# Performance work log

Measured on AMD Instinct MI355X. Metric: run time of the kernel, lower is better.

Reference implementation:

```python
import jax, jax.numpy as jnp
import numpy as np

GRAPH_BIAS_SCALE = 0.7
COMMITMENT_COST = 0.25
DECAY = 0.995
EPS = 1e-6

N_TOKENS = 32768
LATENT = 512
N_SYMBOLS = 8192
EMBED_DIM = 2 * LATENT


def setup_inputs() -> dict:
    key = jax.random.key(0)
    ks = jax.random.split(key, 6)
    return {
        "z_real": jax.random.normal(ks[0], (N_TOKENS, LATENT), jnp.float32),
        "z_imag": jax.random.normal(ks[1], (N_TOKENS, LATENT), jnp.float32),
        "prev_symbol_idx": jax.random.randint(ks[2], (N_TOKENS,), 0, N_SYMBOLS, jnp.int64),
        "codebook": jax.random.normal(ks[3], (N_SYMBOLS, EMBED_DIM), jnp.float32),
        "cluster_size": jax.random.uniform(ks[4], (N_SYMBOLS,), jnp.float32),
        "embed_avg": jax.random.normal(ks[5], (N_SYMBOLS, EMBED_DIM), jnp.float32),
        "adjacency": jax.random.normal(jax.random.fold_in(key, 7), (N_SYMBOLS, N_SYMBOLS), jnp.float32),
    }


def reference(z_real, z_imag, prev_symbol_idx, codebook, cluster_size, embed_avg, adjacency):
    n_symbols = codebook.shape[0]
    z_flat = jnp.concatenate([z_real, z_imag], axis=-1)  # [N, 2*latent]

    # squared-distance matrix via matmul expansion: [N, n_symbols]
    d = (jnp.sum(z_flat ** 2, axis=1, keepdims=True)
         + jnp.sum(codebook ** 2, axis=1)
         - 2.0 * z_flat @ codebook.T)

    # graph-adjacency prior bias (row gather + sigmoid)
    bias = GRAPH_BIAS_SCALE * jax.nn.sigmoid(adjacency[prev_symbol_idx])
    d = d - bias

    min_indices = jnp.argmin(d, axis=1)          # [N]
    z_q = codebook[min_indices]                  # gather, pre-EMA codebook

    # --- EMA codebook update (training mode), scatter via segment_sum ---
    ones = jnp.ones(min_indices.shape, jnp.float32)
    counts = jax.ops.segment_sum(ones, min_indices, num_segments=n_symbols)
    new_cluster_size = cluster_size * DECAY + counts * (1.0 - DECAY)
    embed_sum = jax.ops.segment_sum(jax.lax.stop_gradient(z_flat), min_indices,
                                    num_segments=n_symbols)
    new_embed_avg = embed_avg * DECAY + embed_sum * (1.0 - DECAY)
    n_total = jnp.sum(new_cluster_size)
    cs = (new_cluster_size + EPS) / (n_total + n_symbols * EPS) * n_total
    new_codebook = new_embed_avg / cs[:, None]

    # --- losses and straight-through estimator ---
    loss_vq = jnp.mean((z_q - jax.lax.stop_gradient(z_flat)) ** 2)
    loss_commit = jnp.mean((jax.lax.stop_gradient(z_q) - z_flat) ** 2)
    loss = loss_vq + COMMITMENT_COST * loss_commit

    z_q_st = z_flat + jax.lax.stop_gradient(z_q - z_flat)
    D = z_real.shape[-1]
    z_complex = jax.lax.complex(z_q_st[..., :D], z_q_st[..., D:])

    return z_complex, loss, min_indices, new_codebook, new_cluster_size, new_embed_avg
```

## Files before the change

### kernel.cpp

```cpp
#include <hip/hip_runtime.h>
#include <math.h>
#include <float.h>

#define M_TOK   32768
#define NSYM    8192
#define KDIM    1024
#define LAT     512

#define DECAY_F 0.995f
#define OMD_F   0.005f
#define GBS_F   0.7f
#define EPS_F   1e-6f
#define WIN_F   2.5f
#define LOSS_SCALE (1.25f / 33554432.0f)

typedef unsigned short u16;
typedef unsigned int   u32;
typedef short short8 __attribute__((ext_vector_type(8)));
typedef float f32x4  __attribute__((ext_vector_type(4)));

#define GLOAD_LDS16(g, l) \
    __builtin_amdgcn_global_load_lds((const __attribute__((address_space(1))) u32*)(g), \
                                     (__attribute__((address_space(3))) u32*)(l), 16, 0, 0)

__device__ __forceinline__ u16 f2bf(float f) {
    u32 u = __float_as_uint(f);
    return (u16)((u + 0x7FFF + ((u >> 16) & 1)) >> 16);
}

__global__ void k_conv(const float* __restrict__ zr, const float* __restrict__ zi,
                       const float* __restrict__ cb,
                       u16* __restrict__ A, u16* __restrict__ B,
                       float* __restrict__ cnorm,
                       u32* __restrict__ counts, u32* __restrict__ cursors,
                       u32* __restrict__ qcount, float* __restrict__ out_loss) {
    const int bid = blockIdx.x;
    if (bid < 16384) {
        size_t t = (size_t)bid * 256 + threadIdx.x;
        size_t base = t * 8;
        int tok = (int)(base >> 10);
        int k0  = (int)(base & 1023);
        const float* src = (k0 < 512) ? zr + (size_t)tok * 512 + k0
                                      : zi + (size_t)tok * 512 + (k0 - 512);
        float4 f0 = *(const float4*)src;
        float4 f1 = *(const float4*)(src + 4);
        u32 q0 = f2bf(f0.x) | ((u32)f2bf(f0.y) << 16);
        u32 q1 = f2bf(f0.z) | ((u32)f2bf(f0.w) << 16);
        u32 q2 = f2bf(f1.x) | ((u32)f2bf(f1.y) << 16);
        u32 q3 = f2bf(f1.z) | ((u32)f2bf(f1.w) << 16);
        *(uint4*)&A[base] = make_uint4(q0, q1, q2, q3);
    } else if (bid < 20480) {
        const int b2 = bid - 16384;
        size_t t = (size_t)b2 * 256 + threadIdx.x;
        size_t base = t * 8;
        float4 f0 = *(const float4*)&cb[base];
        float4 f1 = *(const float4*)&cb[base + 4];
        u32 q0 = f2bf(f0.x) | ((u32)f2bf(f0.y) << 16);
        u32 q1 = f2bf(f0.z) | ((u32)f2bf(f0.w) << 16);
        u32 q2 = f2bf(f1.x) | ((u32)f2bf(f1.y) << 16);
        u32 q3 = f2bf(f1.z) | ((u32)f2bf(f1.w) << 16);
        *(uint4*)&B[base] = make_uint4(q0, q1, q2, q3);
        float nrm = f0.x * f0.x + f0.y * f0.y + f0.z * f0.z + f0.w * f0.w
                  + f1.x * f1.x + f1.y * f1.y + f1.z * f1.z + f1.w * f1.w;
#pragma unroll
        for (int m = 32; m; m >>= 1) nrm += __shfl_xor(nrm, m, 64);
        __shared__ float part[4];
        int lane = threadIdx.x & 63, w = threadIdx.x >> 6;
        if (lane == 0) part[w] = nrm;
        __syncthreads();
        if (threadIdx.x == 0)   cnorm[b2 * 2]     = part[0] + part[1];
        if (threadIdx.x == 128) cnorm[b2 * 2 + 1] = part[2] + part[3];
    } else {
        int i = (bid - 20480) * 256 + threadIdx.x;
        if (i < NSYM) { counts[i] = 0; cursors[i] = 0; }
        if (i == 0) { qcount[0] = 0; out_loss[0] = 0.0f; }
    }
}

__global__ __launch_bounds__(256, 4) void k_screen(
    const u16* __restrict__ Ah, const u16* __restrict__ Bh,
    const float* __restrict__ cnorm,
    float* __restrict__ candV, u16* __restrict__ candI)
{
    __shared__ __align__(16) unsigned char smA[16384];
    __shared__ __align__(16) unsigned char smB[16384];
    __shared__ float smv[128][2][2];
    __shared__ float smi[128][2];

    const int sblk = (blockIdx.x & 7) * 128 + (blockIdx.x >> 3);
    const int bx = sblk >> 2;
    const int by = sblk & 3;

    const int tid  = threadIdx.x;
    const int lane = tid & 63;
    const int w    = tid >> 6;
    const int wr   = w >> 1, wc = w & 1;
    const int row0 = bx * 128;
    const int sBase = w * 256;

    for (int cc = 0; cc < 16; ++cc) {
        const int chunk = by * 16 + cc;
        const int colBase = chunk * 128;

        f32x4 acc[4][4];
#pragma unroll
        for (int m = 0; m < 4; ++m)
#pragma unroll
            for (int n = 0; n < 4; ++n) acc[m][n] = (f32x4){0.f, 0.f, 0.f, 0.f};

        for (int ks = 0; ks < 16; ++ks) {
            const int kk0 = ks * 64;
            __syncthreads();
#pragma unroll
            for (int i = 0; i < 4; ++i) {
                int slot = sBase + i * 64 + lane;
                int r = slot >> 3;
                int c = (slot & 7) ^ (r & 7);
                const u16* ga = Ah + ((size_t)(row0 + r) * KDIM + kk0 + c * 8);
                GLOAD_LDS16(ga, smA + (size_t)(sBase + i * 64) * 16);
                const u16* gb = Bh + ((size_t)(colBase + r) * KDIM + kk0 + c * 8);
                GLOAD_LDS16(gb, smB + (size_t)(sBase + i * 64) * 16);
            }
            __syncthreads();
#pragma unroll
            for (int h = 0; h < 2; ++h) {
                short8 af[4], bfr[4];
#pragma unroll
                for (int m = 0; m < 4; ++m) {
                    int r = wr * 64 + m * 16 + (lane & 15);
                    int byte = r * 128 + h * 64 + (lane >> 4) * 16;
                    byte ^= (r & 7) << 4;
                    af[m] = *(const short8*)(smA + byte);
                }
#pragma unroll
                for (int n = 0; n < 4; ++n) {
                    int r = wc * 64 + n * 16 + (lane & 15);
                    int byte = r * 128 + h * 64 + (lane >> 4) * 16;
                    byte ^= (r & 7) << 4;
                    bfr[n] = *(const short8*)(smB + byte);
                }
#pragma unroll
                for (int m = 0; m < 4; ++m)
#pragma unroll
                    for (int n = 0; n < 4; ++n)
                        acc[m][n] = __builtin_amdgcn_mfma_f32_16x16x32_bf16(
                            af[m], bfr[n], acc[m][n], 0, 0, 0);
            }
        }

        float cn[4];
#pragma unroll
        for (int n = 0; n < 4; ++n)
            cn[n] = cnorm[colBase + wc * 64 + n * 16 + (lane & 15)];

#pragma unroll
        for (int m = 0; m < 4; ++m)
#pragma unroll
            for (int j = 0; j < 4; ++j) {
                int rowL = wr * 64 + m * 16 + (lane >> 4) * 4 + j;
                float v1 = INFINITY, v2 = INFINITY, i1v = 0.f;
#pragma unroll
                for (int n = 0; n < 4; ++n) {
                    float s = cn[n] - 2.0f * acc[m][n][j];
                    float ci = (float)(colBase + wc * 64 + n * 16 + (lane & 15));
                    if (s < v1) { v2 = v1; v1 = s; i1v = ci; }
                    else v2 = fminf(v2, s);
                }
#pragma unroll
                for (int msk = 1; msk < 16; msk <<= 1) {
                    float o1 = __shfl_xor(v1, msk, 16);
                    float oi = __shfl_xor(i1v, msk, 16);
                    float o2 = __shfl_xor(v2, msk, 16);
                    float n2 = fminf(fminf(v2, o2), fmaxf(v1, o1));
                    if (o1 < v1) { v1 = o1; i1v = oi; }
                    v2 = n2;
                }
                if ((lane & 15) == 0) {
                    smv[rowL][wc][0] = v1;  smv[rowL][wc][1] = v2;
                    smi[rowL][wc] = i1v;
                }
            }
        __syncthreads();
        {
            int half = tid >> 7;
            int row  = tid & 127;
            float v1 = smv[row][half][0], v2 = smv[row][half][1];
            float iv = smi[row][half];
            size_t tcol = (size_t)(row0 + row);
            int halfIdx = chunk * 2 + half;
            candV[(size_t)(halfIdx * 2 + 0) * M_TOK + tcol] = v1;
            candV[(size_t)(halfIdx * 2 + 1) * M_TOK + tcol] = v2;
            candI[(size_t)halfIdx * M_TOK + tcol]           = (u16)iv;
        }
    }
}

__global__ void k_zero(u32* __restrict__ counts, u32* __restrict__ cursors,
                       u32* __restrict__ qcount, float* __restrict__ out_loss) {
    int i = blockIdx.x * 256 + threadIdx.x;
    if (i < NSYM) { counts[i] = 0; cursors[i] = 0; }
    if (i == 0) { out_loss[0] = 0.0f; qcount[0] = 0; }
}

__device__ __forceinline__ void rescore(
    const float* __restrict__ codebook, const float* __restrict__ adjacency,
    const double* zreg, int prw, int col, int lane, double& bestS, int& bestI)
{
    const float* crow = codebook + (size_t)col * KDIM;
    double dot = 0.0, cn2 = 0.0;
#pragma unroll
    for (int j = 0; j < 16; ++j) {
        double c = (double)crow[lane + 64 * j];
        dot += c * zreg[j]; cn2 += c * c;
    }
#pragma unroll
    for (int m = 32; m; m >>= 1) {
        dot += __shfl_xor(dot, m, 64);
        cn2 += __shfl_xor(cn2, m, 64);
    }
    double a = (double)adjacency[(size_t)prw * NSYM + col];
    double sc = cn2 - 2.0 * dot - (double)GBS_F / (1.0 + exp(-a));
    if (sc < bestS || (sc == bestS && col < bestI)) { bestS = sc; bestI = col; }
}

#define SEL_TOK 32
__global__ __launch_bounds__(256) void k_select(
    const float* __restrict__ zr, const float* __restrict__ zi,
    const int* __restrict__ prev,
    const float* __restrict__ codebook,
    const float* __restrict__ adjacency,
    const float* __restrict__ candV, const u16* __restrict__ candI,
    float* __restrict__ out_idx, u32* __restrict__ counts,
    u32* __restrict__ qcount, u32* __restrict__ queue)
{
    __shared__ float sv[256][SEL_TOK + 1];
    __shared__ u16   si[128][SEL_TOK + 2];
    const int tok0 = blockIdx.x * SEL_TOK;
    const int w = threadIdx.x >> 6, lane = threadIdx.x & 63;

    for (int idx = threadIdx.x; idx < 256 * SEL_TOK; idx += 256) {
        int e = idx >> 5, t = idx & (SEL_TOK - 1);
        sv[e][t] = candV[(size_t)e * M_TOK + tok0 + t];
    }
    for (int idx = threadIdx.x; idx < 128 * SEL_TOK; idx += 256) {
        int e = idx >> 5, t = idx & (SEL_TOK - 1);
        si[e][t] = candI[(size_t)e * M_TOK + tok0 + t];
    }
    __syncthreads();

    for (int tt = 0; tt < SEL_TOK / 4; ++tt) {
        const int t = w * (SEL_TOK / 4) + tt;
        const int tok = tok0 + t;
        float va1 = sv[4 * lane + 0][t];
        float va2 = sv[4 * lane + 1][t];
        float vb1 = sv[4 * lane + 2][t];
        float vb2 = sv[4 * lane + 3][t];
        int   ia  = (int)si[2 * lane + 0][t];
        int   ib  = (int)si[2 * lane + 1][t];

        float mm = fminf(va1, vb1);
#pragma unroll
        for (int m = 32; m; m >>= 1) mm = fminf(mm, __shfl_xor(mm, m, 64));
        const float thr = mm + WIN_F;

        unsigned long long m1a = __ballot(va1 <= thr);
        unsigned long long m1b = __ballot(vb1 <= thr);
        unsigned long long mh  = __ballot(va2 <= thr) | __ballot(vb2 <= thr);

        if (mh != 0) {
            if (lane == 0) { u32 q = atomicAdd(qcount, 1u); queue[q] = (u32)tok; }
        } else if (__popcll(m1a) + __popcll(m1b) == 1) {
            int bestI;
            if (m1a) { int c = __ffsll(m1a) - 1; bestI = __shfl(ia, c, 64); }
            else     { int c = __ffsll(m1b) - 1; bestI = __shfl(ib, c, 64); }
            if (lane == 0) {
                out_idx[tok] = (float)bestI;
                atomicAdd(&counts[bestI], 1u);
            }
        } else {
            double zreg[16];
#pragma unroll
            for (int j = 0; j < 8; ++j)
                zreg[j] = (double)zr[(size_t)tok * LAT + lane + 64 * j];
#pragma unroll
            for (int j = 0; j < 8; ++j)
                zreg[8 + j] = (double)zi[(size_t)tok * LAT + lane + 64 * j];
            const int prw = prev[tok];
            double bestS = DBL_MAX; int bestI = 0x7FFFFFFF;
            unsigned long long sa = m1a, sb = m1b;
            while (sa) { int c = __ffsll(sa) - 1; sa &= sa - 1;
                rescore(codebook, adjacency, zreg, prw, __shfl(ia, c, 64), lane, bestS, bestI); }
            while (sb) { int c = __ffsll(sb) - 1; sb &= sb - 1;
                rescore(codebook, adjacency, zreg, prw, __shfl(ib, c, 64), lane, bestS, bestI); }
            if (lane == 0) {
                out_idx[tok] = (float)bestI;
                atomicAdd(&counts[bestI], 1u);
            }
        }
    }
}

#define MAXC 384
__global__ __launch_bounds__(256) void k_rescan(
    const float* __restrict__ zr, const float* __restrict__ zi,
    const int* __restrict__ prev,
    const float* __restrict__ codebook,
    const float* __restrict__ adjacency,
    const float* __restrict__ candV, const u16* __restrict__ candI,
    const u32* __restrict__ qcount, const u32* __restrict__ queue,
    float* __restrict__ out_idx, u32* __restrict__ counts)
{
    __shared__ double zd[KDIM];
    __shared__ float v1h[128], v2h[128];
    __shared__ u16   i1h[128];
    __shared__ int   collist[MAXC];
    __shared__ int   nsing_sh, nh_sh, scanall_sh;
    __shared__ int   halves[128];
    __shared__ double wsc[4];
    __shared__ int    wix[4];
    __shared__ float  mm_sh;

    const int tid = threadIdx.x;
    const int w = tid >> 6, lane = tid & 63;
    const u32 nq = qcount[0];

    for (u32 qi = blockIdx.x; qi < nq; qi += gridDim.x) {
        const int tok = (int)queue[qi];

        if (tid < 128) {
            v1h[tid] = candV[(size_t)(tid * 2 + 0) * M_TOK + tok];
            v2h[tid] = candV[(size_t)(tid * 2 + 1) * M_TOK + tok];
            i1h[tid] = candI[(size_t)tid * M_TOK + tok];
        }
        for (int k = tid; k < LAT; k += 256) {
            zd[k]       = (double)zr[(size_t)tok * LAT + k];
            zd[LAT + k] = (double)zi[(size_t)tok * LAT + k];
        }
        if (tid == 0) { nsing_sh = 0; nh_sh = 0; scanall_sh = 0; }
        __syncthreads();

        if (tid < 64) {
            float m = fminf(v1h[tid], v1h[tid + 64]);
#pragma unroll
            for (int s = 32; s; s >>= 1) m = fminf(m, __shfl_xor(m, s, 64));
            if (tid == 0) mm_sh = m;
        }
        __syncthreads();
        const float thr = mm_sh + WIN_F;

        if (tid < 128) {
            bool hs = (v2h[tid] <= thr);
            if (hs) { int p = atomicAdd(&nh_sh, 1); halves[p] = tid; }
            else if (v1h[tid] <= thr) { int p = atomicAdd(&nsing_sh, 1); collist[p] = (int)i1h[tid]; }
        }
        __syncthreads();
        int nsing = nsing_sh, nh = nh_sh;
        int nc = nsing + nh * 64;
        if (nc > MAXC) { if (tid == 0) scanall_sh = 1; }
        __syncthreads();
        if (!scanall_sh) {
            for (int h = 0; h < nh; ++h) {
                if (tid < 64) collist[nsing + h * 64 + tid] = halves[h] * 64 + tid;
            }
            nc = nsing + nh * 64;
        }
        __syncthreads();

        const int prw = prev[tok];
        double bestS = DBL_MAX; int bestI = 0x7FFFFFFF;
        const int total = scanall_sh ? NSYM : nc;
        for (int ci = w; ci < total; ci += 4) {
            int col = scanall_sh ? ci : collist[ci];
            const float* crow = codebook + (size_t)col * KDIM;
            double dot = 0.0, cn2 = 0.0;
#pragma unroll
            for (int j = 0; j < 16; ++j) {
                double c = (double)crow[lane + 64 * j];
                dot += c * zd[lane + 64 * j]; cn2 += c * c;
            }
#pragma unroll
            for (int s = 32; s; s >>= 1) {
                dot += __shfl_xor(dot, s, 64);
                cn2 += __shfl_xor(cn2, s, 64);
            }
            double a = (double)adjacency[(size_t)prw * NSYM + col];
            double sc = cn2 - 2.0 * dot - (double)GBS_F / (1.0 + exp(-a));
            if (sc < bestS || (sc == bestS && col < bestI)) { bestS = sc; bestI = col; }
        }
        if (lane == 0) { wsc[w] = bestS; wix[w] = bestI; }
        __syncthreads();
        if (tid == 0) {
            double bs = wsc[0]; int bi = wix[0];
#pragma unroll
            for (int q = 1; q < 4; ++q) {
                if (wsc[q] < bs || (wsc[q] == bs && wix[q] < bi)) { bs = wsc[q]; bi = wix[q]; }
            }
            out_idx[tok] = (float)bi;
            atomicAdd(&counts[bi], 1u);
        }
        __syncthreads();
    }
}

__global__ __launch_bounds__(1024) void k_scan(
    const u32* __restrict__ counts, const float* __restrict__ cs_old,
    float* __restrict__ out_cs, u32* __restrict__ offsets,
    float* __restrict__ scal)
{
    const int tid = threadIdx.x;
    const int lane = tid & 63, w = tid >> 6;
    const int base = tid * 8;
    u32 c[8], pre[8], T = 0;
#pragma unroll
    for (int q = 0; q < 8; ++q) { c[q] = counts[base + q]; pre[q] = T; T += c[q]; }
    u32 inc = T;
#pragma unroll
    for (int d = 1; d < 64; d <<= 1) {
        u32 v = __shfl_up(inc, d, 64);
        if (lane >= d) inc += v;
    }
    __shared__ u32 wt[16];
    if (lane == 63) wt[w] = inc;
    __syncthreads();
    if (tid < 16) {
        u32 v = wt[tid];
#pragma unroll
        for (int d = 1; d < 16; d <<= 1) {
            u32 o = __shfl_up(v, d, 16);
            if (tid >= d) v += o;
        }
        wt[tid] = v;
    }
    __syncthreads();
    u32 ex = (w ? wt[w - 1] : 0) + inc - T;
#pragma unroll
    for (int q = 0; q < 8; ++q) offsets[base + q] = ex + pre[q];

    float nt = 0.0f;
#pragma unroll
    for (int q = 0; q < 8; ++q) {
        float ncs = cs_old[base + q] * DECAY_F + OMD_F * (float)c[q];
        out_cs[base + q] = ncs;
        nt += ncs;
    }
#pragma unroll
    for (int m = 32; m; m >>= 1) nt += __shfl_xor(nt, m, 64);
    __shared__ float red[16];
    if (lane == 0) red[w] = nt;
    __syncthreads();
    if (tid == 0) {
        float s = 0.0f;
#pragma unroll
        for (int i = 0; i < 16; ++i) s += red[i];
        scal[0] = s;
        scal[1] = s + (float)NSYM * EPS_F;
    }
}

__global__ void k_place(const float* __restrict__ idxf, const u32* __restrict__ offsets,
                        u32* __restrict__ cursors, u32* __restrict__ list) {
    int t = blockIdx.x * 256 + threadIdx.x;
    int s = (int)idxf[t];
    u32 slot = atomicAdd(&cursors[s], 1u);
    list[offsets[s] + slot] = (u32)t;
}

__global__ __launch_bounds__(256) void k_emit_fused(
    const float* __restrict__ zr, const float* __restrict__ zi,
    const float* __restrict__ codebook, const float* __restrict__ embed_avg,
    const u32* __restrict__ counts, const u32* __restrict__ offsets,
    const u32* __restrict__ list, const float* __restrict__ out_cs,
    const float* __restrict__ scal,
    float* __restrict__ out_ea, float* __restrict__ out_cb,
    float* __restrict__ out_zc, float* __restrict__ out_loss, int interleaved)
{
    const int s = blockIdx.x;
    const u32 cnt = counts[s], off = offsets[s];
    const int g = threadIdx.x >> 7;
    const int j = (threadIdx.x & 127) * 4;
    float4 cbr = *(const float4*)&codebook[(size_t)s * KDIM + j];
    float4 cbi = *(const float4*)&codebook[(size_t)s * KDIM + LAT + j];
    float ar0 = 0.f, ar1 = 0.f, ar2 = 0.f, ar3 = 0.f;
    float ai0 = 0.f, ai1 = 0.f, ai2 = 0.f, ai3 = 0.f;
    float lsum = 0.f;
    for (u32 n = g; n < cnt; n += 2) {
        int t = (int)list[off + n];
        float4 z0 = *(const float4*)&zr[(size_t)t * LAT + j];
        float4 z1 = *(const float4*)&zi[(size_t)t * LAT + j];
        ar0 += z0.x; ar1 += z0.y; ar2 += z0.z; ar3 += z0.w;
        ai0 += z1.x; ai1 += z1.y; ai2 += z1.z; ai3 += z1.w;
        if (interleaved) {
            float2* dst = (float2*)out_zc + (size_t)t * LAT + j;
            dst[0] = make_float2(cbr.x, cbi.x); dst[1] = make_float2(cbr.y, cbi.y);
            dst[2] = make_float2(cbr.z, cbi.z); dst[3] = make_float2(cbr.w, cbi.w);
        } else {
            *(float4*)&out_zc[(size_t)t * LAT + j] = cbr;
        }
        float d;
        d = cbr.x - z0.x; lsum += d * d;  d = cbr.y - z0.y; lsum += d * d;
        d = cbr.z - z0.z; lsum += d * d;  d = cbr.w - z0.w; lsum += d * d;
        d = cbi.x - z1.x; lsum += d * d;  d = cbi.y - z1.y; lsum += d * d;
        d = cbi.z - z1.z; lsum += d * d;  d = cbi.w - z1.w; lsum += d * d;
    }
    __shared__ float comb[128][8];
    if (g == 1) {
        int r = threadIdx.x & 127;
        comb[r][0] = ar0; comb[r][1] = ar1; comb[r][2] = ar2; comb[r][3] = ar3;
        comb[r][4] = ai0; comb[r][5] = ai1; comb[r][6] = ai2; comb[r][7] = ai3;
    }
    __syncthreads();
    if (g == 0) {
        int r = threadIdx.x;
        ar0 += comb[r][0]; ar1 += comb[r][1]; ar2 += comb[r][2]; ar3 += comb[r][3];
        ai0 += comb[r][4]; ai1 += comb[r][5]; ai2 += comb[r][6]; ai3 += comb[r][7];
        float4 ea0 = *(const float4*)&embed_avg[(size_t)s * KDIM + j];
        float4 ea1 = *(const float4*)&embed_avg[(size_t)s * KDIM + LAT + j];
        float4 ner = make_float4(ea0.x * DECAY_F + ar0 * OMD_F, ea0.y * DECAY_F + ar1 * OMD_F,
                                 ea0.z * DECAY_F + ar2 * OMD_F, ea0.w * DECAY_F + ar3 * OMD_F);
        float4 nei = make_float4(ea1.x * DECAY_F + ai0 * OMD_F, ea1.y * DECAY_F + ai1 * OMD_F,
                                 ea1.z * DECAY_F + ai2 * OMD_F, ea1.w * DECAY_F + ai3 * OMD_F);
        *(float4*)&out_ea[(size_t)s * KDIM + j]       = ner;
        *(float4*)&out_ea[(size_t)s * KDIM + LAT + j] = nei;
        float ntot = scal[0], denom = scal[1];
        float cs = (out_cs[s] + EPS_F) / denom * ntot;
        float inv = 1.0f / cs;
        *(float4*)&out_cb[(size_t)s * KDIM + j] =
            make_float4(ner.x * inv, ner.y * inv, ner.z * inv, ner.w * inv);
        *(float4*)&out_cb[(size_t)s * KDIM + LAT + j] =
            make_float4(nei.x * inv, nei.y * inv, nei.z * inv, nei.w * inv);
    }
#pragma unroll
    for (int m = 32; m; m >>= 1) lsum += __shfl_xor(lsum, m, 64);
    __shared__ float red[4];
    int wv = threadIdx.x >> 6, lane = threadIdx.x & 63;
    if (lane == 0) red[wv] = lsum;
    __syncthreads();
    if (threadIdx.x == 0)
        atomicAdd(out_loss, (red[0] + red[1] + red[2] + red[3]) * LOSS_SCALE);
}

__global__ __launch_bounds__(256) void k_emit(
    const float* __restrict__ zr, const float* __restrict__ zi,
    const float* __restrict__ embed_avg,
    const u32* __restrict__ counts, const u32* __restrict__ offsets,
    const u32* __restrict__ list, const float* __restrict__ out_cs,
    const float* __restrict__ scal,
    float* __restrict__ out_ea, float* __restrict__ out_cb)
{
    const int s = blockIdx.x;
    const u32 cnt = counts[s], off = offsets[s];
    const int j = threadIdx.x * 4;
    float a0 = 0.f, a1 = 0.f, a2 = 0.f, a3 = 0.f;
    for (u32 n = 0; n < cnt; ++n) {
        int t = (int)list[off + n];
        const float* src = (j < 512) ? zr + (size_t)t * 512 + j
                                     : zi + (size_t)t * 512 + (j - 512);
        float4 v = *(const float4*)src;
        a0 += v.x; a1 += v.y; a2 += v.z; a3 += v.w;
    }
    float4 ea = *(const float4*)&embed_avg[(size_t)s * KDIM + j];
    float4 nea = make_float4(ea.x * DECAY_F + a0 * OMD_F,
                             ea.y * DECAY_F + a1 * OMD_F,
                             ea.z * DECAY_F + a2 * OMD_F,
                             ea.w * DECAY_F + a3 * OMD_F);
    *(float4*)&out_ea[(size_t)s * KDIM + j] = nea;
    float ntot = scal[0], denom = scal[1];
    float cs = (out_cs[s] + EPS_F) / denom * ntot;
    float inv = 1.0f / cs;
    *(float4*)&out_cb[(size_t)s * KDIM + j] =
        make_float4(nea.x * inv, nea.y * inv, nea.z * inv, nea.w * inv);
}

__global__ __launch_bounds__(256) void k_zq(
    const float* __restrict__ zr, const float* __restrict__ zi,
    const float* __restrict__ codebook, const float* __restrict__ idxf,
    float* __restrict__ out_zc, float* __restrict__ out_loss, int interleaved)
{
    const int w = threadIdx.x >> 6, lane = threadIdx.x & 63;
    const int tok = blockIdx.x * 4 + w;
    const int mi = (int)idxf[tok];
    const int j0 = lane * 8;
    float4 re0 = *(const float4*)&codebook[(size_t)mi * KDIM + j0];
    float4 re1 = *(const float4*)&codebook[(size_t)mi * KDIM + j0 + 4];
    float4 im0 = *(const float4*)&codebook[(size_t)mi * KDIM + LAT + j0];
    float4 im1 = *(const float4*)&codebook[(size_t)mi * KDIM + LAT + j0 + 4];
    float4 zr0 = *(const float4*)&zr[(size_t)tok * LAT + j0];
    float4 zr1 = *(const float4*)&zr[(size_t)tok * LAT + j0 + 4];
    float4 zi0 = *(const float4*)&zi[(size_t)tok * LAT + j0];
    float4 zi1 = *(const float4*)&zi[(size_t)tok * LAT + j0 + 4];
    if (interleaved) {
        float2* dst = (float2*)out_zc + (size_t)tok * LAT + j0;
        dst[0] = make_float2(re0.x, im0.x); dst[1] = make_float2(re0.y, im0.y);
        dst[2] = make_float2(re0.z, im0.z); dst[3] = make_float2(re0.w, im0.w);
        dst[4] = make_float2(re1.x, im1.x); dst[5] = make_float2(re1.y, im1.y);
        dst[6] = make_float2(re1.z, im1.z); dst[7] = make_float2(re1.w, im1.w);
    } else {
        *(float4*)&out_zc[(size_t)tok * LAT + j0]     = re0;
        *(float4*)&out_zc[(size_t)tok * LAT + j0 + 4] = re1;
    }
    float l = 0.f;
    l += (re0.x-zr0.x)*(re0.x-zr0.x) + (re0.y-zr0.y)*(re0.y-zr0.y)
       + (re0.z-zr0.z)*(re0.z-zr0.z) + (re0.w-zr0.w)*(re0.w-zr0.w);
    l += (re1.x-zr1.x)*(re1.x-zr1.x) + (re1.y-zr1.y)*(re1.y-zr1.y)
       + (re1.z-zr1.z)*(re1.z-zr1.z) + (re1.w-zr1.w)*(re1.w-zr1.w);
    l += (im0.x-zi0.x)*(im0.x-zi0.x) + (im0.y-zi0.y)*(im0.y-zi0.y)
       + (im0.z-zi0.z)*(im0.z-zi0.z) + (im0.w-zi0.w)*(im0.w-zi0.w);
    l += (im1.x-zi1.x)*(im1.x-zi1.x) + (im1.y-zi1.y)*(im1.y-zi1.y)
       + (im1.z-zi1.z)*(im1.z-zi1.z) + (im1.w-zi1.w)*(im1.w-zi1.w);
#pragma unroll
    for (int m = 32; m; m >>= 1) l += __shfl_xor(l, m, 64);
    if (lane == 0) atomicAdd(out_loss, l * LOSS_SCALE);
}

extern "C" void kernel_launch(void* const* d_in, const int* in_sizes, int n_in,
                              void* d_out, int out_size, void* d_ws, size_t ws_size,
                              hipStream_t stream) {
    const float* z_real     = (const float*)d_in[0];
    const float* z_imag     = (const float*)d_in[1];
    const int*   prev_idx   = (const int*)d_in[2];
    const float* codebook   = (const float*)d_in[3];
    const float* cluster_sz = (const float*)d_in[4];
    const float* embed_avg  = (const float*)d_in[5];
    const float* adjacency  = (const float*)d_in[6];

    float* out = (float*)d_out;

    const size_t REST = 1 + (size_t)M_TOK + (size_t)NSYM * KDIM + NSYM
                      + (size_t)NSYM * KDIM;
    size_t zc_n = (size_t)out_size - REST;
    const size_t n_z = (size_t)M_TOK * LAT;
    int interleaved = (zc_n >= 2 * n_z) ? 1 : 0;

    float* out_zc   = out;
    float* out_loss = out + zc_n;
    float* out_idx  = out + zc_n + 1;
    float* out_cb   = out + zc_n + 1 + M_TOK;
    float* out_cs   = out_cb + (size_t)NSYM * KDIM;
    float* out_ea   = out_cs + NSYM;

    u16*   A_hi  = (u16*)out_zc;
    u16*   B_hi  = (u16*)out_cb;
    float* cnorm = out_cb + 4194304;
    float* candV = out_ea;
    u16*   candI = (u16*)(out_cb + 4202496);

    const size_t WS_NEED = (size_t)(NSYM * 3 + M_TOK * 2 + 8) * 4;
    int use_ws = (ws_size >= WS_NEED) ? 1 : 0;
    u32 *counts, *cursors, *offsets, *list, *qcount, *queue;
    float* scal;
    if (use_ws) {
        u32* wsp = (u32*)d_ws;
        counts  = wsp;             cursors = counts + NSYM;
        offsets = cursors + NSYM;  list    = offsets + NSYM;
        queue   = list + M_TOK;
        scal    = (float*)(queue + M_TOK);
        qcount  = (u32*)(scal + 2);
    } else {
        counts  = (u32*)out_zc;    cursors = counts + NSYM;
        offsets = cursors + NSYM;  list    = offsets + NSYM;
        scal    = (float*)(list + M_TOK);
        qcount  = (u32*)(scal + 2);
        queue   = qcount + 1;
    }

    k_conv<<<use_ws ? 20512 : 20480, 256, 0, stream>>>(z_real, z_imag, codebook,
                                                       A_hi, B_hi, cnorm,
                                                       counts, cursors, qcount,
                                                       out_loss);
    k_screen<<<1024, 256, 0, stream>>>(A_hi, B_hi, cnorm, candV, candI);
    if (!use_ws)
        k_zero<<<32, 256, 0, stream>>>(counts, cursors, qcount, out_loss);
    k_select<<<M_TOK / SEL_TOK, 256, 0, stream>>>(z_real, z_imag, prev_idx,
                                                  codebook, adjacency,
                                                  candV, candI, out_idx, counts,
                                                  qcount, queue);
    k_rescan<<<256, 256, 0, stream>>>(z_real, z_imag, prev_idx, codebook,
                                      adjacency, candV, candI,
                                      qcount, queue, out_idx, counts);
    k_scan<<<1, 1024, 0, stream>>>(counts, cluster_sz, out_cs, offsets, scal);
    k_place<<<M_TOK / 256, 256, 0, stream>>>(out_idx, offsets, cursors, list);
    if (use_ws) {
        k_emit_fused<<<NSYM, 256, 0, stream>>>(z_real, z_imag, codebook, embed_avg,
                                               counts, offsets, list, out_cs, scal,
                                               out_ea, out_cb, out_zc, out_loss,
                                               interleaved);
    } else {
        k_emit<<<NSYM, 256, 0, stream>>>(z_real, z_imag, embed_avg, counts, offsets,
                                         list, out_cs, scal, out_ea, out_cb);
        k_zq<<<M_TOK / 4, 256, 0, stream>>>(z_real, z_imag, codebook, out_idx,
                                            out_zc, out_loss, interleaved);
    }
}
```

Measured before the change: 1.205 ms.

## Triple-buffer LDS ring with async prefetch in screening GEMM

Replaces the single-buffer load/sync/compute loop in k_screen with a 3-slot LDS ring of 32-wide K tiles. Each stage is prefetched two steps ahead across chunk boundaries, gated by vmcnt waits and a single barrier per step. This is meant to overlap global-to-LDS loads with the MFMA work instead of stalling on every tile. In exchange it halves the K per step (more barriers), changes the swizzle, and drops the occupancy hint from launch_bounds.

```diff
diff --git a/kernel.cpp b/kernel.cpp
--- a/kernel.cpp
+++ b/kernel.cpp
@@ -77,13 +77,13 @@
     }
 }
 
-__global__ __launch_bounds__(256, 4) void k_screen(
+__global__ __launch_bounds__(256) void k_screen(
     const u16* __restrict__ Ah, const u16* __restrict__ Bh,
     const float* __restrict__ cnorm,
     float* __restrict__ candV, u16* __restrict__ candI)
 {
-    __shared__ __align__(16) unsigned char smA[16384];
-    __shared__ __align__(16) unsigned char smB[16384];
+    __shared__ __align__(16) unsigned char ringA[3][8192];
+    __shared__ __align__(16) unsigned char ringB[3][8192];
     __shared__ float smv[128][2][2];
     __shared__ float smi[128][2];
 
@@ -96,58 +96,66 @@
     const int w    = tid >> 6;
     const int wr   = w >> 1, wc = w & 1;
     const int row0 = bx * 128;
-    const int sBase = w * 256;
+
+    auto stage = [&](int g, int ri) {
+        const int chunk = by * 16 + (g >> 5);
+        const int kk0 = (g & 31) * 32;
+#pragma unroll
+        for (int i = 0; i < 2; ++i) {
+            int slotBase = i * 256 + w * 64;
+            int slot = slotBase + lane;
+            int r = slot >> 2;
+            int c = (slot & 3) ^ (r & 3);
+            const u16* ga = Ah + (((size_t)(row0 + r)) << 10) + kk0 + c * 8;
+            GLOAD_LDS16(ga, ringA[ri] + slotBase * 16);
+            const u16* gb = Bh + (((size_t)(chunk * 128 + r)) << 10) + kk0 + c * 8;
+            GLOAD_LDS16(gb, ringB[ri] + slotBase * 16);
+        }
+    };
+
+    stage(0, 0);
+    stage(1, 1);
+    int bi = 0;
 
     for (int cc = 0; cc < 16; ++cc) {
+        f32x4 acc[4][4];
+#pragma unroll
+        for (int m = 0; m < 4; ++m)
+#pragma unroll
+            for (int n = 0; n < 4; ++n) acc[m][n] = (f32x4){0.f, 0.f, 0.f, 0.f};
+
+        for (int ks = 0; ks < 32; ++ks) {
+            const int g = cc * 32 + ks;
+            asm volatile("s_waitcnt vmcnt(4)" ::: "memory");
+            __builtin_amdgcn_s_barrier();
+            if (g + 2 < 512) {
+                int bi2 = bi + 2; if (bi2 >= 3) bi2 -= 3;
+                stage(g + 2, bi2);
+            }
+            short8 af[4], bfr[4];
+#pragma unroll
+            for (int m = 0; m < 4; ++m) {
+                int r = wr * 64 + m * 16 + (lane & 15);
+                int gg = (lane >> 4) ^ (r & 3);
+                af[m] = *(const short8*)(ringA[bi] + r * 64 + gg * 16);
+            }
+#pragma unroll
+            for (int n = 0; n < 4; ++n) {
+                int r = wc * 64 + n * 16 + (lane & 15);
+                int gg = (lane >> 4) ^ (r & 3);
+                bfr[n] = *(const short8*)(ringB[bi] + r * 64 + gg * 16);
+            }
+#pragma unroll
+            for (int m = 0; m < 4; ++m)
+#pragma unroll
+                for (int n = 0; n < 4; ++n)
+                    acc[m][n] = __builtin_amdgcn_mfma_f32_16x16x32_bf16(
+                        af[m], bfr[n], acc[m][n], 0, 0, 0);
+            ++bi; if (bi == 3) bi = 0;
+        }
+
         const int chunk = by * 16 + cc;
         const int colBase = chunk * 128;
-
-        f32x4 acc[4][4];
-#pragma unroll
-        for (int m = 0; m < 4; ++m)
-#pragma unroll
-            for (int n = 0; n < 4; ++n) acc[m][n] = (f32x4){0.f, 0.f, 0.f, 0.f};
-
-        for (int ks = 0; ks < 16; ++ks) {
-            const int kk0 = ks * 64;
-            __syncthreads();
-#pragma unroll
-            for (int i = 0; i < 4; ++i) {
-                int slot = sBase + i * 64 + lane;
-                int r = slot >> 3;
-                int c = (slot & 7) ^ (r & 7);
-                const u16* ga = Ah + ((size_t)(row0 + r) * KDIM + kk0 + c * 8);
-                GLOAD_LDS16(ga, smA + (size_t)(sBase + i * 64) * 16);
-                const u16* gb = Bh + ((size_t)(colBase + r) * KDIM + kk0 + c * 8);
-                GLOAD_LDS16(gb, smB + (size_t)(sBase + i * 64) * 16);
-            }
-            __syncthreads();
-#pragma unroll
-            for (int h = 0; h < 2; ++h) {
-                short8 af[4], bfr[4];
-#pragma unroll
-                for (int m = 0; m < 4; ++m) {
-                    int r = wr * 64 + m * 16 + (lane & 15);
-                    int byte = r * 128 + h * 64 + (lane >> 4) * 16;
-                    byte ^= (r & 7) << 4;
-                    af[m] = *(const short8*)(smA + byte);
-                }
-#pragma unroll
-                for (int n = 0; n < 4; ++n) {
-                    int r = wc * 64 + n * 16 + (lane & 15);
-                    int byte = r * 128 + h * 64 + (lane >> 4) * 16;
-                    byte ^= (r & 7) << 4;
-                    bfr[n] = *(const short8*)(smB + byte);
-                }
-#pragma unroll
-                for (int m = 0; m < 4; ++m)
-#pragma unroll
-                    for (int n = 0; n < 4; ++n)
-                        acc[m][n] = __builtin_amdgcn_mfma_f32_16x16x32_bf16(
-                            af[m], bfr[n], acc[m][n], 0, 0, 0);
-            }
-        }
-
         float cn[4];
 #pragma unroll
         for (int n = 0; n < 4; ++n)
@@ -192,6 +200,7 @@
             candV[(size_t)(halfIdx * 2 + 1) * M_TOK + tcol] = v2;
             candI[(size_t)halfIdx * M_TOK + tcol]           = (u16)iv;
         }
+        __syncthreads();
     }
 }
 
```

Result: slower. 1.550 ms (+28.6%).

## Double-buffer LDS tiles in screening GEMM to overlap global loads with MFMA

Applied to the files above, without the earlier changes.

Converts the k_screen bf16 GEMM main loop to a double-buffered LDS scheme. The next K-slice, including the next column chunk, is prefetched with global_load_lds into the alternate buffer before computing on the current one, using an explicit vmcnt wait and raw s_barriers. This targets load latency that was previously exposed between two syncthreads per step. LDS use doubles to 64KB and the launch-bounds occupancy hint of 4 is dropped, so fewer blocks may fit per CU.

```diff
diff --git a/kernel.cpp b/kernel.cpp
--- a/kernel.cpp
+++ b/kernel.cpp
@@ -77,13 +77,13 @@
     }
 }
 
-__global__ __launch_bounds__(256, 4) void k_screen(
+__global__ __launch_bounds__(256) void k_screen(
     const u16* __restrict__ Ah, const u16* __restrict__ Bh,
     const float* __restrict__ cnorm,
     float* __restrict__ candV, u16* __restrict__ candI)
 {
-    __shared__ __align__(16) unsigned char smA[16384];
-    __shared__ __align__(16) unsigned char smB[16384];
+    __shared__ __align__(16) unsigned char smA[2][16384];
+    __shared__ __align__(16) unsigned char smB[2][16384];
     __shared__ float smv[128][2][2];
     __shared__ float smi[128][2];
 
@@ -98,6 +98,23 @@
     const int row0 = bx * 128;
     const int sBase = w * 256;
 
+    auto stage = [&](int g, int ri) {
+        const int kk0 = (g & 15) * 64;
+        const int colB = (by * 16 + (g >> 4)) * 128;
+#pragma unroll
+        for (int i = 0; i < 4; ++i) {
+            int slot = sBase + i * 64 + lane;
+            int r = slot >> 3;
+            int c = (slot & 7) ^ (r & 7);
+            const u16* ga = Ah + ((size_t)(row0 + r) * KDIM + kk0 + c * 8);
+            GLOAD_LDS16(ga, smA[ri] + (size_t)(sBase + i * 64) * 16);
+            const u16* gb = Bh + ((size_t)(colB + r) * KDIM + kk0 + c * 8);
+            GLOAD_LDS16(gb, smB[ri] + (size_t)(sBase + i * 64) * 16);
+        }
+    };
+
+    stage(0, 0);
+
     for (int cc = 0; cc < 16; ++cc) {
         const int chunk = by * 16 + cc;
         const int colBase = chunk * 128;
@@ -109,19 +126,17 @@
             for (int n = 0; n < 4; ++n) acc[m][n] = (f32x4){0.f, 0.f, 0.f, 0.f};
 
         for (int ks = 0; ks < 16; ++ks) {
-            const int kk0 = ks * 64;
-            __syncthreads();
-#pragma unroll
-            for (int i = 0; i < 4; ++i) {
-                int slot = sBase + i * 64 + lane;
-                int r = slot >> 3;
-                int c = (slot & 7) ^ (r & 7);
-                const u16* ga = Ah + ((size_t)(row0 + r) * KDIM + kk0 + c * 8);
-                GLOAD_LDS16(ga, smA + (size_t)(sBase + i * 64) * 16);
-                const u16* gb = Bh + ((size_t)(colBase + r) * KDIM + kk0 + c * 8);
-                GLOAD_LDS16(gb, smB + (size_t)(sBase + i * 64) * 16);
-            }
-            __syncthreads();
+            const int g = cc * 16 + ks;
+            const int bi = g & 1;
+            if (g + 1 < 256) {
+                stage(g + 1, bi ^ 1);
+                asm volatile("s_waitcnt vmcnt(8)" ::: "memory");
+            } else {
+                asm volatile("s_waitcnt vmcnt(0)" ::: "memory");
+            }
+            __builtin_amdgcn_sched_barrier(0);
+            __builtin_amdgcn_s_barrier();
+            __builtin_amdgcn_sched_barrier(0);
 #pragma unroll
             for (int h = 0; h < 2; ++h) {
                 short8 af[4], bfr[4];
@@ -130,14 +145,14 @@
                     int r = wr * 64 + m * 16 + (lane & 15);
                     int byte = r * 128 + h * 64 + (lane >> 4) * 16;
                     byte ^= (r & 7) << 4;
-                    af[m] = *(const short8*)(smA + byte);
+                    af[m] = *(const short8*)(smA[bi] + byte);
                 }
 #pragma unroll
                 for (int n = 0; n < 4; ++n) {
                     int r = wc * 64 + n * 16 + (lane & 15);
                     int byte = r * 128 + h * 64 + (lane >> 4) * 16;
                     byte ^= (r & 7) << 4;
-                    bfr[n] = *(const short8*)(smB + byte);
+                    bfr[n] = *(const short8*)(smB[bi] + byte);
                 }
 #pragma unroll
                 for (int m = 0; m < 4; ++m)
@@ -146,6 +161,8 @@
                         acc[m][n] = __builtin_amdgcn_mfma_f32_16x16x32_bf16(
                             af[m], bfr[n], acc[m][n], 0, 0, 0);
             }
+            __builtin_amdgcn_sched_barrier(0);
+            __builtin_amdgcn_s_barrier();
         }
 
         float cn[4];
@@ -192,6 +209,7 @@
             candV[(size_t)(halfIdx * 2 + 1) * M_TOK + tcol] = v2;
             candI[(size_t)halfIdx * M_TOK + tcol]           = (u16)iv;
         }
+        __syncthreads();
     }
 }
 
```

Result: slower. 1.300 ms (+7.9%).
